# Kernel optimization log

Measured on AMD Instinct MI355X. Metric: run time of the kernel, lower is better.

## Reference

```python
import jax, jax.numpy as jnp
import numpy as np

DIM = 1024
NUM_HEADS = 16
HD = DIM // NUM_HEADS  # 64
ROPE_DIM = 64
ROPE_BASE = 10000.0


def setup_inputs() -> dict:
    key = jax.random.key(0)
    ks = jax.random.split(key, 5)
    B, N = 2, 2048
    s = 0.02
    return {
        "x": jax.random.normal(ks[0], (B, N, DIM), dtype=jnp.float32),
        "qkv_w": jax.random.normal(ks[1], (3 * DIM, DIM), dtype=jnp.float32) * s,
        "qkv_b": jax.random.normal(ks[2], (3 * DIM,), dtype=jnp.float32) * s,
        "proj_w": jax.random.normal(ks[3], (DIM, DIM), dtype=jnp.float32) * s,
        "proj_b": jax.random.normal(ks[4], (DIM,), dtype=jnp.float32) * s,
    }


def _apply_rope(t):
    # t: [B, H, N, D] with D even; interleaved (even, odd) pair rotation
    D = t.shape[-1]
    N = t.shape[2]
    pos = jnp.arange(N, dtype=t.dtype)
    inv = 1.0 / (ROPE_BASE ** (jnp.arange(0, D, 2, dtype=t.dtype) / D))
    freqs = pos[:, None] * inv[None, :]          # [N, D/2]
    cos = jnp.cos(freqs)[None, None]             # [1,1,N,D/2]
    sin = jnp.sin(freqs)[None, None]
    e = t[..., 0::2]
    o = t[..., 1::2]
    eo = e * cos - o * sin
    oo = e * sin + o * cos
    return jnp.stack([eo, oo], axis=-1).reshape(t.shape)


def reference(x, qkv_w, qkv_b, proj_w, proj_b):
    B, N, C = x.shape
    H, D = NUM_HEADS, HD
    scale = D ** -0.5
    qkv = x @ qkv_w.T + qkv_b                     # [B,N,3C]
    qkv = qkv.reshape(B, N, 3, H, D).transpose(2, 0, 3, 1, 4)  # [3,B,H,N,D]
    q, k, v = qkv[0], qkv[1], qkv[2]
    # RoPE on first ROPE_DIM dims of each head (here ROPE_DIM == HD)
    q = jnp.concatenate([_apply_rope(q[..., :ROPE_DIM]), q[..., ROPE_DIM:]], axis=-1)
    k = jnp.concatenate([_apply_rope(k[..., :ROPE_DIM]), k[..., ROPE_DIM:]], axis=-1)
    attn = jnp.einsum('bhnd,bhmd->bhnm', q, k) * scale
    attn = jax.nn.softmax(attn, axis=-1)
    out = jnp.einsum('bhnm,bhmd->bhnd', attn, v)  # [B,H,N,D]
    out = out.transpose(0, 2, 1, 3).reshape(B, N, C)
    return out @ proj_w.T + proj_b
```

## Files before the change

### kernel.cpp

```cpp
#include <hip/hip_runtime.h>
#include <hip/hip_bf16.h>
#include <stdint.h>

#define DIM   1024
#define NH    16
#define HDIM  64
#define SEQ   2048
#define BATCH 2
#define BHN   32
#define MTOK  4096
#define SC2   0.18033688f

using u16 = unsigned short;
using u32 = unsigned int;
typedef __attribute__((ext_vector_type(8))) short short8;
typedef __attribute__((ext_vector_type(4))) float f32x4;
typedef __attribute__((ext_vector_type(16))) float f32x16;

__device__ __forceinline__ u16 f2bf(float f) {
  __hip_bfloat16 h = __float2bfloat16(f);
  return *reinterpret_cast<u16*>(&h);
}
__device__ __forceinline__ u32 pk2(float lo, float hi) {
  return (u32)f2bf(lo) | ((u32)f2bf(hi) << 16);
}
__device__ __forceinline__ u32 cvtpk(float lo, float hi) {
  u32 r;
  asm("v_cvt_pk_bf16_f32 %0, %1, %2" : "=v"(r) : "v"(lo), "v"(hi));
  return r;
}
__device__ __forceinline__ float vexp2(float x) {
  float r;
  asm("v_exp_f32 %0, %1" : "=v"(r) : "v"(x));
  return r;
}

__device__ __forceinline__ void gload16(const void* g, void* lds) {
  __builtin_amdgcn_global_load_lds(
      (const __attribute__((address_space(1))) u32*)g,
      (__attribute__((address_space(3))) u32*)lds, 16, 0, 0);
}

#define PREP_A 1048576
#define PREP_B 1835008
#define PREP_C 2097152
#define PREP_E 2162688
__global__ void k_prep(const float4* __restrict__ x, const float4* __restrict__ qw,
                       const float4* __restrict__ pw, ushort4* __restrict__ xb,
                       ushort4* __restrict__ qwb, ushort4* __restrict__ pwb,
                       float2* __restrict__ tab) {
  int i = blockIdx.x * blockDim.x + threadIdx.x;
  if (i < PREP_A) {
    float4 v = x[i];
    xb[i] = make_ushort4(f2bf(v.x), f2bf(v.y), f2bf(v.z), f2bf(v.w));
  } else if (i < PREP_B) {
    int j = i - PREP_A;
    float4 v = qw[j];
    qwb[j] = make_ushort4(f2bf(v.x), f2bf(v.y), f2bf(v.z), f2bf(v.w));
  } else if (i < PREP_C) {
    int j = i - PREP_B;
    float4 v = pw[j];
    pwb[j] = make_ushort4(f2bf(v.x), f2bf(v.y), f2bf(v.z), f2bf(v.w));
  } else if (i < PREP_E) {
    int j = i - PREP_C;
    int n = j >> 5, f = j & 31;
    float inv = powf(10000.f, -(2.f * f) / 64.f);
    float s, c;
    sincosf((float)n * inv, &s, &c);
    tab[j] = make_float2(c, s);
  }
}

template <int EPI>
__global__ __launch_bounds__(256, 2) void k_gemm(
    const u16* __restrict__ A, const u16* __restrict__ Bt,
    const float* __restrict__ bias, int K,
    float* __restrict__ out_f, u16* __restrict__ qb, u16* __restrict__ kb,
    u16* __restrict__ vtb, const float2* __restrict__ tab) {
  __shared__ u16 As[128 * 64];
  __shared__ u16 Bs[128 * 64];
  const int tid = threadIdx.x;
  const int wid = tid >> 6, lane = tid & 63;
  const int lq = lane & 15, g = lane >> 4;
  const int wr = wid >> 1, wc = wid & 1;
  const int brow = blockIdx.y * 128;
  const int bcol = blockIdx.x * 128;
  f32x4 acc[4][4] = {};
  const u16* Ab = A + (size_t)brow * K;
  const u16* Bb = Bt + (size_t)bcol * K;

  for (int k0 = 0; k0 < K; k0 += 64) {
#pragma unroll
    for (int t = 0; t < 4; t++) {
      int rl = wid * 32 + t * 8 + (lane >> 3);
      int cs = (lane & 7) ^ (rl & 7);
      gload16(Ab + (size_t)rl * K + k0 + cs * 8, &As[(wid * 32 + t * 8) * 64]);
      gload16(Bb + (size_t)rl * K + k0 + cs * 8, &Bs[(wid * 32 + t * 8) * 64]);
    }
    __syncthreads();
#pragma unroll
    for (int kc = 0; kc < 2; kc++) {
      short8 af[4], bfr[4];
#pragma unroll
      for (int mt = 0; mt < 4; mt++) {
        int r = wr * 64 + mt * 16 + lq;
        af[mt] = *reinterpret_cast<const short8*>(&As[r * 64 + (((kc * 4 + g) ^ (r & 7)) * 8)]);
      }
#pragma unroll
      for (int nt = 0; nt < 4; nt++) {
        int r = wc * 64 + nt * 16 + lq;
        bfr[nt] = *reinterpret_cast<const short8*>(&Bs[r * 64 + (((kc * 4 + g) ^ (r & 7)) * 8)]);
      }
#pragma unroll
      for (int mt = 0; mt < 4; mt++)
#pragma unroll
        for (int nt = 0; nt < 4; nt++)
          acc[mt][nt] = __builtin_amdgcn_mfma_f32_16x16x32_bf16(af[mt], bfr[nt], acc[mt][nt], 0, 0, 0);
    }
    __syncthreads();
  }

#pragma unroll
  for (int mt = 0; mt < 4; mt++) {
    int row0 = brow + wr * 64 + mt * 16 + g * 4;
#pragma unroll
    for (int nt = 0; nt < 4; nt++) {
      int col = bcol + wc * 64 + nt * 16 + lq;
      float bv = bias[col];
      float v[4];
#pragma unroll
      for (int r = 0; r < 4; r++) v[r] = acc[mt][nt][r] + bv;
      if (EPI == 0) {
#pragma unroll
        for (int r = 0; r < 4; r++) out_f[(size_t)(row0 + r) * DIM + col] = v[r];
      } else {
        int which = col >> 10, hd = col & 1023, hdh = hd >> 6, d = hd & 63;
        int bb = row0 >> 11, n0 = row0 & 2047;
        int bh = bb * NH + hdh;
        if (which == 2) {
          uint2 pv = make_uint2(pk2(v[0], v[1]), pk2(v[2], v[3]));
          size_t idx = ((((size_t)bh * 32 + (n0 >> 6)) * 8 + ((n0 >> 3) & 7)) * 64 + d) * 8 + (n0 & 7);
          *reinterpret_cast<uint2*>(&vtb[idx]) = pv;
        } else {
#pragma unroll
          for (int r = 0; r < 4; r++) {
            int n = n0 + r;
            float p = __shfl_xor(v[r], 1);
            float2 cs = tab[n * 32 + (d >> 1)];
            float vv = (d & 1) ? fmaf(p, cs.y, v[r] * cs.x)
                               : fmaf(-p, cs.y, v[r] * cs.x);
            if (which == 0) {
              qb[((size_t)bh * SEQ + n) * HDIM + d] = f2bf(vv * SC2);
            } else {
              size_t idx = ((((size_t)bh * 32 + (n >> 6)) * 8 + (d >> 3)) * 64 + (n & 63)) * 8 + (d & 7);
              kb[idx] = f2bf(vv);
            }
          }
        }
      }
    }
  }
}

__global__ __launch_bounds__(256) void k_attn(
    const u16* __restrict__ qg, const u16* __restrict__ kg,
    const u16* __restrict__ vg, u16* __restrict__ aout) {
  const int tid = threadIdx.x;
  const int wid = tid >> 6, lane = tid & 63;
  const int l31 = lane & 31, h = lane >> 5;

  const int bid = blockIdx.x;
  const int xcd = bid & 7, slot = bid >> 3;
  const int bh = xcd * 4 + (slot >> 4);
  const int qt = slot & 15;
  const int b = bh >> 4, hh = bh & 15;
  const int q0 = qt * 128 + wid * 32;

  const u16* kb0 = kg + (size_t)bh * SEQ * HDIM + h * 512 + l31 * 8;
  const u16* vb0 = vg + (size_t)bh * SEQ * HDIM + h * 512 + l31 * 8;

  const u16* qrow = qg + ((size_t)bh * SEQ + q0 + l31) * HDIM;
  short8 qf[4];
#pragma unroll
  for (int c = 0; c < 4; c++)
    qf[c] = *reinterpret_cast<const short8*>(qrow + c * 16 + h * 8);

  short8 ones;
#pragma unroll
  for (int i = 0; i < 8; i++) ones[i] = (short)0x3F80;

  short8 kf[8], vf[8];
  f32x16 sA0, sA1, sB0, sB1;
  f32x16 oA = {}, oB = {}, ls = {};

  auto loadKfull = [&](int t) {
    const u16* kn = kb0 + (size_t)t * 4096;
#pragma unroll
    for (int c = 0; c < 4; c++) {
      kf[2 * c]     = *reinterpret_cast<const short8*>(kn + c * 1024);
      kf[2 * c + 1] = *reinterpret_cast<const short8*>(kn + c * 1024 + 256);
    }
  };
  auto loadVfull = [&](int t) {
    const u16* vn = vb0 + (size_t)t * 4096;
#pragma unroll
    for (int c = 0; c < 4; c++) {
      vf[2 * c]     = *reinterpret_cast<const short8*>(vn + c * 1024);
      vf[2 * c + 1] = *reinterpret_cast<const short8*>(vn + c * 1024 + 256);
    }
  };

  auto step = [&](f32x16& sc0, f32x16& sc1, f32x16& sn0, f32x16& sn1,
                  const u16* knxt, const u16* vnxt, bool doQK, bool doK) {
#pragma unroll
    for (int c = 0; c < 4; c++) {
      f32x16& sv = (c < 2) ? sc0 : sc1;
      const int e0 = (c & 1) * 8;
      float e[8];
#pragma unroll
      for (int j = 0; j < 8; j++) e[j] = vexp2(sv[e0 + j]);
      u32 a0 = cvtpk(e[0], e[1]), a1 = cvtpk(e[2], e[3]);
      u32 b0 = cvtpk(e[4], e[5]), b1 = cvtpk(e[6], e[7]);
      auto r0 = __builtin_amdgcn_permlane32_swap(a0, b0, false, false);
      auto r1 = __builtin_amdgcn_permlane32_swap(a1, b1, false, false);
      union { u32 u[4]; short8 v; } pp;
      pp.u[0] = r0[0]; pp.u[1] = r1[0]; pp.u[2] = r0[1]; pp.u[3] = r1[1];
      short8 pf = pp.v;

      __builtin_amdgcn_s_setprio(1);
      oA = __builtin_amdgcn_mfma_f32_32x32x16_bf16(vf[2 * c],     pf, oA, 0, 0, 0);
      oB = __builtin_amdgcn_mfma_f32_32x32x16_bf16(vf[2 * c + 1], pf, oB, 0, 0, 0);
      ls = __builtin_amdgcn_mfma_f32_32x32x16_bf16(ones,          pf, ls, 0, 0, 0);
      if (doQK) {
        if (c == 0) {
          f32x16 z = {};
          sn0 = __builtin_amdgcn_mfma_f32_32x32x16_bf16(kf[0], qf[0], z, 0, 0, 0);
          sn1 = __builtin_amdgcn_mfma_f32_32x32x16_bf16(kf[1], qf[0], z, 0, 0, 0);
        } else {
          sn0 = __builtin_amdgcn_mfma_f32_32x32x16_bf16(kf[2 * c],     qf[c], sn0, 0, 0, 0);
          sn1 = __builtin_amdgcn_mfma_f32_32x32x16_bf16(kf[2 * c + 1], qf[c], sn1, 0, 0, 0);
        }
      }
      __builtin_amdgcn_s_setprio(0);

      if (doK) {
        kf[2 * c]     = *reinterpret_cast<const short8*>(knxt + c * 1024);
        kf[2 * c + 1] = *reinterpret_cast<const short8*>(knxt + c * 1024 + 256);
      }
      vf[2 * c]     = *reinterpret_cast<const short8*>(vnxt + c * 1024);
      vf[2 * c + 1] = *reinterpret_cast<const short8*>(vnxt + c * 1024 + 256);
    }
  };

  loadKfull(0);
  loadVfull(0);
  {
    f32x16 z = {};
    sA0 = z; sA1 = z;
#pragma unroll
    for (int c = 0; c < 4; c++) {
      sA0 = __builtin_amdgcn_mfma_f32_32x32x16_bf16(kf[2 * c],     qf[c], sA0, 0, 0, 0);
      sA1 = __builtin_amdgcn_mfma_f32_32x32x16_bf16(kf[2 * c + 1], qf[c], sA1, 0, 0, 0);
    }
  }
  loadKfull(1);

#pragma unroll 1
  for (int i = 0; i < 15; i++) {
    const u16* kA = kb0 + (size_t)(2 * i + 2) * 4096;
    const u16* vA = vb0 + (size_t)(2 * i + 1) * 4096;
    step(sA0, sA1, sB0, sB1, kA, vA, true, true);
    const u16* kB = kb0 + (size_t)(2 * i + 3) * 4096;
    const u16* vB = vb0 + (size_t)(2 * i + 2) * 4096;
    step(sB0, sB1, sA0, sA1, kB, vB, true, true);
  }
  const u16* v31 = vb0 + (size_t)31 * 4096;
  step(sA0, sA1, sB0, sB1, kb0, v31, true, false);
  step(sB0, sB1, sA0, sA1, kb0, v31, false, false);

  float invl = 1.0f / ls[0];
  int n = q0 + l31;
  u16* op = aout + ((size_t)(b * SEQ + n)) * DIM + hh * HDIM;
#pragma unroll
  for (int g = 0; g < 4; g++) {
    u32 w0 = pk2(oA[4 * g] * invl, oA[4 * g + 1] * invl);
    u32 w1 = pk2(oA[4 * g + 2] * invl, oA[4 * g + 3] * invl);
    *reinterpret_cast<uint2*>(op + 8 * g + 4 * h) = make_uint2(w0, w1);
    u32 x0 = pk2(oB[4 * g] * invl, oB[4 * g + 1] * invl);
    u32 x1 = pk2(oB[4 * g + 2] * invl, oB[4 * g + 3] * invl);
    *reinterpret_cast<uint2*>(op + 32 + 8 * g + 4 * h) = make_uint2(x0, x1);
  }
}

extern "C" void kernel_launch(void* const* d_in, const int* in_sizes, int n_in,
                              void* d_out, int out_size, void* d_ws, size_t ws_size,
                              hipStream_t stream) {
  (void)in_sizes; (void)n_in; (void)out_size; (void)ws_size;
  const float* x      = (const float*)d_in[0];
  const float* qkv_w  = (const float*)d_in[1];
  const float* qkv_b  = (const float*)d_in[2];
  const float* proj_w = (const float*)d_in[3];
  const float* proj_b = (const float*)d_in[4];
  float* out = (float*)d_out;

  char* w = (char*)d_ws;
  u16* xb     = (u16*)w;  w += (size_t)MTOK * DIM * 2;
  u16* wqkvb  = (u16*)w;  w += (size_t)3 * DIM * DIM * 2;
  u16* wprojb = (u16*)w;  w += (size_t)DIM * DIM * 2;
  u16* qb     = (u16*)w;  w += (size_t)BHN * SEQ * HDIM * 2;
  u16* kb     = (u16*)w;  w += (size_t)BHN * SEQ * HDIM * 2;
  u16* vtb    = (u16*)w;  w += (size_t)BHN * SEQ * HDIM * 2;
  u16* aout   = (u16*)w;  w += (size_t)MTOK * DIM * 2;
  float2* tab = (float2*)w;

  k_prep<<<(PREP_E + 255) / 256, 256, 0, stream>>>(
      (const float4*)x, (const float4*)qkv_w, (const float4*)proj_w,
      (ushort4*)xb, (ushort4*)wqkvb, (ushort4*)wprojb, tab);

  k_gemm<1><<<dim3(3 * DIM / 128, MTOK / 128), 256, 0, stream>>>(
      xb, wqkvb, qkv_b, DIM, nullptr, qb, kb, vtb, tab);

  k_attn<<<512, 256, 0, stream>>>(qb, kb, vtb, aout);

  k_gemm<0><<<dim3(DIM / 128, MTOK / 128), 256, 0, stream>>>(
      aout, wprojb, proj_b, DIM, out, nullptr, nullptr, nullptr, nullptr);
}
```

Baseline: 126.7 us.

## Stage K/V tiles through a 4-buffer LDS ring with async global loads

Each block's four waves now cooperatively copy K and V tiles into a 64KB shared-memory ring using direct global-to-LDS loads, instead of each wave loading the full K/V tiles into registers. Fragments are then read from LDS, with prefetch two tiles ahead and vmcnt waits plus barriers per tile. This is meant to cut the fourfold redundant global/L2 traffic across waves and reduce register pressure. In exchange it adds block-wide barriers and a large LDS footprint that limits occupancy.

```diff
diff --git a/kernel.cpp b/kernel.cpp
--- a/kernel.cpp
+++ b/kernel.cpp
@@ -165,6 +165,7 @@
 __global__ __launch_bounds__(256) void k_attn(
     const u16* __restrict__ qg, const u16* __restrict__ kg,
     const u16* __restrict__ vg, u16* __restrict__ aout) {
+  __shared__ __align__(16) char smem[65536];
   const int tid = threadIdx.x;
   const int wid = tid >> 6, lane = tid & 63;
   const int l31 = lane & 31, h = lane >> 5;
@@ -176,8 +177,8 @@
   const int b = bh >> 4, hh = bh & 15;
   const int q0 = qt * 128 + wid * 32;
 
-  const u16* kb0 = kg + (size_t)bh * SEQ * HDIM + h * 512 + l31 * 8;
-  const u16* vb0 = vg + (size_t)bh * SEQ * HDIM + h * 512 + l31 * 8;
+  const u16* kbase = kg + (size_t)bh * SEQ * HDIM;
+  const u16* vbase = vg + (size_t)bh * SEQ * HDIM;
 
   const u16* qrow = qg + ((size_t)bh * SEQ + q0 + l31) * HDIM;
   short8 qf[4];
@@ -189,31 +190,56 @@
 #pragma unroll
   for (int i = 0; i < 8; i++) ones[i] = (short)0x3F80;
 
-  short8 kf[8], vf[8];
+  int koff[4];
+#pragma unroll
+  for (int c = 0; c < 4; c++)
+    koff[c] = (2 * c + h) * 1024 + l31 * 16;
+
   f32x16 sA0, sA1, sB0, sB1;
   f32x16 oA = {}, oB = {}, ls = {};
 
-  auto loadKfull = [&](int t) {
-    const u16* kn = kb0 + (size_t)t * 4096;
+  auto stage = [&](int buf, int tidx) {
+    char* kd = smem + buf * 16384;
+    const u16* kt = kbase + (size_t)tidx * 4096 + lane * 8;
+    const u16* vt = vbase + (size_t)tidx * 4096 + lane * 8;
+#pragma unroll
+    for (int i = 0; i < 2; i++) {
+      int g = wid + i * 4;
+      gload16(kt + g * 512, kd + g * 1024);
+      gload16(vt + g * 512, kd + 8192 + g * 1024);
+    }
+  };
+
+  const int NT = SEQ / 64;
+
+  auto body = [&](f32x16& sc0, f32x16& sc1, f32x16& sn0, f32x16& sn1, int t, bool last) {
+    if (!last) asm volatile("s_waitcnt vmcnt(4)" ::: "memory");
+    else       asm volatile("s_waitcnt vmcnt(0)" ::: "memory");
+    __builtin_amdgcn_s_barrier();
+
+    const char* kbp = smem + (t & 3) * 16384;
+    const char* vbp = smem + ((t - 1) & 3) * 16384 + 8192;
+
 #pragma unroll
     for (int c = 0; c < 4; c++) {
-      kf[2 * c]     = *reinterpret_cast<const short8*>(kn + c * 1024);
-      kf[2 * c + 1] = *reinterpret_cast<const short8*>(kn + c * 1024 + 256);
-    }
-  };
-  auto loadVfull = [&](int t) {
-    const u16* vn = vb0 + (size_t)t * 4096;
-#pragma unroll
-    for (int c = 0; c < 4; c++) {
-      vf[2 * c]     = *reinterpret_cast<const short8*>(vn + c * 1024);
-      vf[2 * c + 1] = *reinterpret_cast<const short8*>(vn + c * 1024 + 256);
-    }
-  };
-
-  auto step = [&](f32x16& sc0, f32x16& sc1, f32x16& sn0, f32x16& sn1,
-                  const u16* knxt, const u16* vnxt, bool doQK, bool doK) {
-#pragma unroll
-    for (int c = 0; c < 4; c++) {
+      short8 kf0 = *reinterpret_cast<const short8*>(kbp + koff[c]);
+      short8 kf1 = *reinterpret_cast<const short8*>(kbp + koff[c] + 512);
+      __builtin_amdgcn_s_setprio(1);
+      if (c == 0) {
+        f32x16 z = {};
+        sn0 = __builtin_amdgcn_mfma_f32_32x32x16_bf16(kf0, qf[0], z, 0, 0, 0);
+        sn1 = __builtin_amdgcn_mfma_f32_32x32x16_bf16(kf1, qf[0], z, 0, 0, 0);
+      } else {
+        sn0 = __builtin_amdgcn_mfma_f32_32x32x16_bf16(kf0, qf[c], sn0, 0, 0, 0);
+        sn1 = __builtin_amdgcn_mfma_f32_32x32x16_bf16(kf1, qf[c], sn1, 0, 0, 0);
+      }
+      __builtin_amdgcn_s_setprio(0);
+
+      if (c == 0 && t + 2 < NT) stage((t + 2) & 3, t + 2);
+
+      short8 vf0 = *reinterpret_cast<const short8*>(vbp + koff[c]);
+      short8 vf1 = *reinterpret_cast<const short8*>(vbp + koff[c] + 512);
+
       f32x16& sv = (c < 2) ? sc0 : sc1;
       const int e0 = (c & 1) * 8;
       float e[8];
@@ -228,55 +254,63 @@
       short8 pf = pp.v;
 
       __builtin_amdgcn_s_setprio(1);
-      oA = __builtin_amdgcn_mfma_f32_32x32x16_bf16(vf[2 * c],     pf, oA, 0, 0, 0);
-      oB = __builtin_amdgcn_mfma_f32_32x32x16_bf16(vf[2 * c + 1], pf, oB, 0, 0, 0);
-      ls = __builtin_amdgcn_mfma_f32_32x32x16_bf16(ones,          pf, ls, 0, 0, 0);
-      if (doQK) {
-        if (c == 0) {
-          f32x16 z = {};
-          sn0 = __builtin_amdgcn_mfma_f32_32x32x16_bf16(kf[0], qf[0], z, 0, 0, 0);
-          sn1 = __builtin_amdgcn_mfma_f32_32x32x16_bf16(kf[1], qf[0], z, 0, 0, 0);
-        } else {
-          sn0 = __builtin_amdgcn_mfma_f32_32x32x16_bf16(kf[2 * c],     qf[c], sn0, 0, 0, 0);
-          sn1 = __builtin_amdgcn_mfma_f32_32x32x16_bf16(kf[2 * c + 1], qf[c], sn1, 0, 0, 0);
-        }
-      }
+      oA = __builtin_amdgcn_mfma_f32_32x32x16_bf16(vf0,  pf, oA, 0, 0, 0);
+      oB = __builtin_amdgcn_mfma_f32_32x32x16_bf16(vf1,  pf, oB, 0, 0, 0);
+      ls = __builtin_amdgcn_mfma_f32_32x32x16_bf16(ones, pf, ls, 0, 0, 0);
       __builtin_amdgcn_s_setprio(0);
-
-      if (doK) {
-        kf[2 * c]     = *reinterpret_cast<const short8*>(knxt + c * 1024);
-        kf[2 * c + 1] = *reinterpret_cast<const short8*>(knxt + c * 1024 + 256);
-      }
-      vf[2 * c]     = *reinterpret_cast<const short8*>(vnxt + c * 1024);
-      vf[2 * c + 1] = *reinterpret_cast<const short8*>(vnxt + c * 1024 + 256);
     }
   };
 
-  loadKfull(0);
-  loadVfull(0);
+  stage(0, 0);
+  stage(1, 1);
+  asm volatile("s_waitcnt vmcnt(4)" ::: "memory");
+  __builtin_amdgcn_s_barrier();
   {
+    const char* kbp = smem;
     f32x16 z = {};
     sA0 = z; sA1 = z;
 #pragma unroll
     for (int c = 0; c < 4; c++) {
-      sA0 = __builtin_amdgcn_mfma_f32_32x32x16_bf16(kf[2 * c],     qf[c], sA0, 0, 0, 0);
-      sA1 = __builtin_amdgcn_mfma_f32_32x32x16_bf16(kf[2 * c + 1], qf[c], sA1, 0, 0, 0);
-    }
-  }
-  loadKfull(1);
+      short8 kf0 = *reinterpret_cast<const short8*>(kbp + koff[c]);
+      short8 kf1 = *reinterpret_cast<const short8*>(kbp + koff[c] + 512);
+      __builtin_amdgcn_s_setprio(1);
+      sA0 = __builtin_amdgcn_mfma_f32_32x32x16_bf16(kf0, qf[c], sA0, 0, 0, 0);
+      sA1 = __builtin_amdgcn_mfma_f32_32x32x16_bf16(kf1, qf[c], sA1, 0, 0, 0);
+      __builtin_amdgcn_s_setprio(0);
+      if (c == 0) stage(2, 2);
+    }
+  }
 
 #pragma unroll 1
   for (int i = 0; i < 15; i++) {
-    const u16* kA = kb0 + (size_t)(2 * i + 2) * 4096;
-    const u16* vA = vb0 + (size_t)(2 * i + 1) * 4096;
-    step(sA0, sA1, sB0, sB1, kA, vA, true, true);
-    const u16* kB = kb0 + (size_t)(2 * i + 3) * 4096;
-    const u16* vB = vb0 + (size_t)(2 * i + 2) * 4096;
-    step(sB0, sB1, sA0, sA1, kB, vB, true, true);
-  }
-  const u16* v31 = vb0 + (size_t)31 * 4096;
-  step(sA0, sA1, sB0, sB1, kb0, v31, true, false);
-  step(sB0, sB1, sA0, sA1, kb0, v31, false, false);
+    body(sA0, sA1, sB0, sB1, 2 * i + 1, false);
+    body(sB0, sB1, sA0, sA1, 2 * i + 2, false);
+  }
+  body(sA0, sA1, sB0, sB1, 31, true);
+
+  {
+    const char* vbp = smem + 3 * 16384 + 8192;
+#pragma unroll
+    for (int c = 0; c < 4; c++) {
+      short8 vf0 = *reinterpret_cast<const short8*>(vbp + koff[c]);
+      short8 vf1 = *reinterpret_cast<const short8*>(vbp + koff[c] + 512);
+      f32x16& sv = (c < 2) ? sB0 : sB1;
+      const int e0 = (c & 1) * 8;
+      float e[8];
+#pragma unroll
+      for (int j = 0; j < 8; j++) e[j] = vexp2(sv[e0 + j]);
+      u32 a0 = cvtpk(e[0], e[1]), a1 = cvtpk(e[2], e[3]);
+      u32 b0 = cvtpk(e[4], e[5]), b1 = cvtpk(e[6], e[7]);
+      auto r0 = __builtin_amdgcn_permlane32_swap(a0, b0, false, false);
+      auto r1 = __builtin_amdgcn_permlane32_swap(a1, b1, false, false);
+      union { u32 u[4]; short8 v; } pp;
+      pp.u[0] = r0[0]; pp.u[1] = r1[0]; pp.u[2] = r0[1]; pp.u[3] = r1[1];
+      short8 pf = pp.v;
+      oA = __builtin_amdgcn_mfma_f32_32x32x16_bf16(vf0,  pf, oA, 0, 0, 0);
+      oB = __builtin_amdgcn_mfma_f32_32x32x16_bf16(vf1,  pf, oB, 0, 0, 0);
+      ls = __builtin_amdgcn_mfma_f32_32x32x16_bf16(ones, pf, ls, 0, 0, 0);
+    }
+  }
 
   float invl = 1.0f / ls[0];
   int n = q0 + l31;
```

Measured after the change: 123.2 us. 1.03x faster.
